# Kernel optimization log

Hardware: AMD Instinct MI355X
Metric: run time of the kernel (lower is better)

## Reference

```python
import jax, jax.numpy as jnp
import numpy as np

N0, N1, N2 = 65536, 8192, 1024   # node counts per depth (pool factor 8, as in original m1*2=8)
DEG = 6                          # avg degree of k-space neighbor graphs
K = 10                           # number of Gaussian kernels in GMMConv


def _pool_graph(n_fine):
    # bidirectional edges between each group of 8 nodes and its representative (last node of group)
    mem = jnp.arange(n_fine)
    rep = (mem // 8) * 8 + 7
    return jnp.concatenate([mem, rep]), jnp.concatenate([rep, mem])


def setup_inputs() -> dict:
    key = jax.random.key(0)
    ks = list(jax.random.split(key, 40))
    E1, E2, E3 = DEG * N0, DEG * N1, DEG * N2
    d = {}
    d['n_feat'] = jax.random.normal(ks[0], (N0, 2), jnp.float32)
    d['src1'] = jax.random.randint(ks[1], (E1,), 0, N0)
    d['dst1'] = jax.random.randint(ks[2], (E1,), 0, N0)
    d['pkor1'] = 0.5 * jax.random.normal(ks[3], (E1, 2), jnp.float32)
    d['src2'] = jax.random.randint(ks[4], (E2,), 0, N1)
    d['dst2'] = jax.random.randint(ks[5], (E2,), 0, N1)
    d['pkor2'] = 0.5 * jax.random.normal(ks[6], (E2, 2), jnp.float32)
    d['src3'] = jax.random.randint(ks[7], (E3,), 0, N2)
    d['dst3'] = jax.random.randint(ks[8], (E3,), 0, N2)
    d['pkor3'] = 0.5 * jax.random.normal(ks[9], (E3, 2), jnp.float32)
    d['pm1_src'], d['pm1_dst'] = _pool_graph(N0)
    d['pm2_src'], d['pm2_dst'] = _pool_graph(N1)
    d['idx1'] = jnp.arange(N1) * 8 + 7
    d['idx2'] = jnp.arange(N2) * 8 + 7

    def lin(k, fi, fo):
        return jax.random.normal(k, (fi, K * fo), jnp.float32) / np.float32(np.sqrt(fi * K))

    d['W1'] = lin(ks[10], 2, 32)
    d['mu1'] = jax.random.normal(ks[11], (K, 2), jnp.float32)
    d['is1'] = jax.random.uniform(ks[12], (K, 2), jnp.float32, 0.5, 1.5)
    d['b1'] = 0.01 * jax.random.normal(ks[13], (32,), jnp.float32)
    d['W2'] = lin(ks[14], 32, 64)
    d['mu2'] = jax.random.normal(ks[15], (K, 2), jnp.float32)
    d['is2'] = jax.random.uniform(ks[16], (K, 2), jnp.float32, 0.5, 1.5)
    d['W3'] = lin(ks[17], 64, 128)
    d['mu3'] = jax.random.normal(ks[18], (K, 2), jnp.float32)
    d['is3'] = jax.random.uniform(ks[19], (K, 2), jnp.float32, 0.5, 1.5)
    d['W4'] = lin(ks[20], 192, 64)
    d['mu4'] = jax.random.normal(ks[21], (K, 2), jnp.float32)
    d['is4'] = jax.random.uniform(ks[22], (K, 2), jnp.float32, 0.5, 1.5)
    d['W5'] = lin(ks[23], 96, 40)
    d['mu5'] = jax.random.normal(ks[24], (K, 2), jnp.float32)
    d['is5'] = jax.random.uniform(ks[25], (K, 2), jnp.float32, 0.5, 1.5)
    d['b5'] = 0.01 * jax.random.normal(ks[26], (40,), jnp.float32)
    return d


def gmm_conv(x, W, mu, inv_sigma, src, dst, pseudo, n, bias=None):
    # DGL GMMConv, aggregator 'mean': h=fc(x) -> (N,K,F); gaussian edge weights over 2D pseudo coords
    h = (x @ W).reshape(x.shape[0], K, -1)                                   # (N,K,F)
    diff = pseudo[:, None, :] - mu[None, :, :]                               # (E,K,2)
    gw = jnp.exp(-0.5 * jnp.sum(diff * diff * (inv_sigma[None] ** 2), -1))   # (E,K)
    msg = h[src] * gw[:, :, None]                                            # (E,K,F)
    s = jax.ops.segment_sum(msg, dst, num_segments=n)
    deg = jax.ops.segment_sum(jnp.ones(dst.shape, x.dtype), dst, num_segments=n)
    out = jnp.sum(s / jnp.maximum(deg, 1.0)[:, None, None], axis=1)          # mean over edges, sum over kernels
    return out if bias is None else out + bias


def max_reduce(h, src, dst, n):
    # DGL update_all(copy_u, max): nodes with no in-edges get 0
    m = jax.ops.segment_max(h[src], dst, num_segments=n)
    deg = jax.ops.segment_sum(jnp.ones(dst.shape, h.dtype), dst, num_segments=n)
    return jnp.where(deg[:, None] > 0, m, jnp.zeros((), h.dtype))


def reference(n_feat, src1, dst1, pkor1, src2, dst2, pkor2, src3, dst3, pkor3,
              pm1_src, pm1_dst, pm2_src, pm2_dst, idx1, idx2,
              W1, mu1, is1, b1, W2, mu2, is2, W3, mu3, is3,
              W4, mu4, is4, W5, mu5, is5, b5):
    # encoder
    out0 = jax.nn.relu(gmm_conv(n_feat, W1, mu1, is1, src1, dst1, pkor1, N0, b1))      # (N0,32) skip0
    h = max_reduce(out0, pm1_src, pm1_dst, N0)[idx1]                                    # MaxPool -> (N1,32)
    out1 = jax.nn.relu(gmm_conv(h, W2, mu2, is2, src2, dst2, pkor2, N1))                # (N1,64) skip1
    h = max_reduce(out1, pm2_src, pm2_dst, N1)[idx2]                                    # MaxPool -> (N2,64)
    out2 = jax.nn.relu(gmm_conv(h, W3, mu3, is3, src3, dst3, pkor3, N2))                # (N2,128) bottleneck
    # decoder
    hu = jnp.zeros((N1, out2.shape[1]), out2.dtype).at[idx2].set(out2)
    hu = max_reduce(hu, pm2_src, pm2_dst, N1)                                           # UpSample -> (N1,128)
    out3 = jax.nn.relu(gmm_conv(jnp.concatenate([hu, out1], 1), W4, mu4, is4,
                                src2, dst2, pkor2, N1))                                 # (N1,64)
    hu = jnp.zeros((N0, out3.shape[1]), out3.dtype).at[idx1].set(out3)
    hu = max_reduce(hu, pm1_src, pm1_dst, N0)                                           # UpSample -> (N0,64)
    return jnp.tanh(gmm_conv(jnp.concatenate([hu, out0], 1), W5, mu5, is5,
                             src1, dst1, pkor1, N0, b5))                                # (N0,40)
```

## Files before the change

### kernel.cpp

```cpp
#include <hip/hip_runtime.h>


#define N0C 65536
#define N1C 8192
#define N2C 1024
#define KK 10

typedef _Float16 half2t __attribute__((ext_vector_type(2)));
typedef _Float16 half4 __attribute__((ext_vector_type(4)));
typedef _Float16 f16x8 __attribute__((ext_vector_type(8)));
typedef float f32x4 __attribute__((ext_vector_type(4)));

static inline int cdiv(long long a, long long b) { return (int)((a + b - 1) / b); }

__device__ __forceinline__ size_t fragi(int r, int kd, int KDT) {
    return ((size_t)(r >> 4) * KDT + (kd >> 5)) * 64 + ((kd >> 3) & 3) * 16 + (r & 15);
}


__global__ __launch_bounds__(256)
void k_hist3(const int* __restrict__ d1, const int* __restrict__ d2,
             const int* __restrict__ d3, int* __restrict__ g1,
             int* __restrict__ g2, int* __restrict__ g3,
             int E1, int E2, int E3) {
    int i = blockIdx.x * 256 + threadIdx.x;
    if (i < E1) atomicAdd(&g1[d1[i]], 1);
    else if (i < E1 + E2) atomicAdd(&g2[d2[i - E1]], 1);
    else if (i < E1 + E2 + E3) atomicAdd(&g3[d3[i - E1 - E2]], 1);
}

__device__ __forceinline__ void map_graph(int b, int& lb, int& gi) {
    if (b < 256) { gi = 0; lb = b; }
    else if (b < 288) { gi = 1; lb = b - 256; }
    else { gi = 2; lb = b - 288; }
}

__global__ __launch_bounds__(256)
void k_scanall(const int* __restrict__ deg1, int* __restrict__ off1, float* __restrict__ inv1,
               const int* __restrict__ deg2, int* __restrict__ off2, float* __restrict__ inv2,
               const int* __restrict__ deg3, int* __restrict__ off3, float* __restrict__ inv3,
               int E1, int E2, int E3) {
    __shared__ int s[256];
    int lb, gi; map_graph(blockIdx.x, lb, gi);
    const int* deg = gi == 0 ? deg1 : (gi == 1 ? deg2 : deg3);
    int* off = gi == 0 ? off1 : (gi == 1 ? off2 : off3);
    float* inv = gi == 0 ? inv1 : (gi == 1 ? inv2 : inv3);
    int n = gi == 0 ? N0C : (gi == 1 ? N1C : N2C);
    int E = gi == 0 ? E1 : (gi == 1 ? E2 : E3);
    int pre = 0;
    for (int i = threadIdx.x; i < lb * 256; i += 256) pre += deg[i];
    s[threadIdx.x] = pre;
    __syncthreads();
#pragma unroll
    for (int d = 128; d > 0; d >>= 1) {
        if (threadIdx.x < d) s[threadIdx.x] += s[threadIdx.x + d];
        __syncthreads();
    }
    int base = s[0];
    __syncthreads();
    int i = lb * 256 + threadIdx.x;
    int v = deg[i];
    s[threadIdx.x] = v;
    __syncthreads();
#pragma unroll
    for (int d = 1; d < 256; d <<= 1) {
        int t = (threadIdx.x >= d) ? s[threadIdx.x - d] : 0;
        __syncthreads();
        s[threadIdx.x] += t;
        __syncthreads();
    }
    off[i] = base + s[threadIdx.x] - v;
    inv[i] = 1.0f / fmaxf((float)v, 1.0f);
    if (i == n - 1) off[n] = E;
}

__global__ __launch_bounds__(256)
void k_scatter3(const int* __restrict__ s1, const int* __restrict__ d1,
                const float* __restrict__ p1, const int* __restrict__ o1,
                int* __restrict__ c1, int* __restrict__ cs1, float2* __restrict__ cp1,
                const int* __restrict__ s2, const int* __restrict__ d2,
                const float* __restrict__ p2, const int* __restrict__ o2,
                int* __restrict__ c2, int* __restrict__ cs2, float2* __restrict__ cp2,
                const int* __restrict__ s3, const int* __restrict__ d3,
                const float* __restrict__ p3, const int* __restrict__ o3,
                int* __restrict__ c3, int* __restrict__ cs3, float2* __restrict__ cp3,
                int E1, int E2, int E3) {
    int i = blockIdx.x * 256 + threadIdx.x;
    const int* src; const int* dst; const float* pk; const int* off;
    int* cur; int* csrc; float2* cpk; int e;
    if (i < E1) { src = s1; dst = d1; pk = p1; off = o1; cur = c1; csrc = cs1; cpk = cp1; e = i; }
    else if (i < E1 + E2) { src = s2; dst = d2; pk = p2; off = o2; cur = c2; csrc = cs2; cpk = cp2; e = i - E1; }
    else if (i < E1 + E2 + E3) { src = s3; dst = d3; pk = p3; off = o3; cur = c3; csrc = cs3; cpk = cp3; e = i - E1 - E2; }
    else return;
    int d = dst[e];
    int p = off[d] + atomicAdd(&cur[d], 1);
    csrc[p] = src[e];
    cpk[p] = reinterpret_cast<const float2*>(pk)[e];
}

__global__ __launch_bounds__(256)
void k_gw(const float2* __restrict__ cp1, const float2* __restrict__ cp2,
          const float2* __restrict__ cp3,
          const float* __restrict__ mu1, const float* __restrict__ is1,
          const float* __restrict__ mu5, const float* __restrict__ is5,
          const float* __restrict__ mu2, const float* __restrict__ is2,
          const float* __restrict__ mu4, const float* __restrict__ is4,
          const float* __restrict__ mu3, const float* __restrict__ is3,
          float* __restrict__ g1, float* __restrict__ g5, float* __restrict__ g2,
          float* __restrict__ g4, float* __restrict__ g3,
          int E1, int E2, int E3) {
    int i = blockIdx.x * 256 + threadIdx.x;
    const float2* cp; const float* mu; const float* isg; float* g; int e;
    if (i < E1) { cp = cp1; mu = mu1; isg = is1; g = g1; e = i; }
    else if (i < 2 * E1) { cp = cp1; mu = mu5; isg = is5; g = g5; e = i - E1; }
    else if (i < 2 * E1 + E2) { cp = cp2; mu = mu2; isg = is2; g = g2; e = i - 2 * E1; }
    else if (i < 2 * E1 + 2 * E2) { cp = cp2; mu = mu4; isg = is4; g = g4; e = i - 2 * E1 - E2; }
    else if (i < 2 * E1 + 2 * E2 + E3) { cp = cp3; mu = mu3; isg = is3; g = g3; e = i - 2 * E1 - 2 * E2; }
    else return;
    float2 pk = cp[e];
    float o[KK];
#pragma unroll
    for (int k = 0; k < KK; ++k) {
        float dx = (pk.x - mu[2 * k]) * isg[2 * k];
        float dy = (pk.y - mu[2 * k + 1]) * isg[2 * k + 1];
        o[k] = __expf(-0.5f * (dx * dx + dy * dy));
    }
    float4* gp = reinterpret_cast<float4*>(g + (size_t)e * 12);
    gp[0] = make_float4(o[0], o[1], o[2], o[3]);
    gp[1] = make_float4(o[4], o[5], o[6], o[7]);
    gp[2] = make_float4(o[8], o[9], 0.f, 0.f);
}

#define LOAD_G2(gwp, j, G)                                                   \
    {                                                                        \
        const float4* gp_ = reinterpret_cast<const float4*>((gwp) + (size_t)(j) * 12); \
        float4 g0_ = gp_[0], g1_ = gp_[1];                                   \
        float2 g2_ = *reinterpret_cast<const float2*>(gp_ + 2);              \
        G[0] = g0_.x; G[1] = g0_.y; G[2] = g0_.z; G[3] = g0_.w;              \
        G[4] = g1_.x; G[5] = g1_.y; G[6] = g1_.z; G[7] = g1_.w;              \
        G[8] = g2_.x; G[9] = g2_.y;                                          \
    }

__global__ __launch_bounds__(256)
void k_prep_wt(const float* __restrict__ W1, const float* __restrict__ W2,
               const float* __restrict__ W3, const float* __restrict__ W4,
               const float* __restrict__ W5,
               _Float16* __restrict__ T2,
               _Float16* __restrict__ T3, _Float16* __restrict__ T4,
               _Float16* __restrict__ T5, int* __restrict__ degs, int degn) {
    int id = blockIdx.x * 256 + threadIdx.x;
    if (id < degn) degs[id] = 0;
    if (id < 20480) {
        int f = id / 320, kc = id % 320;
        T2[fragi(f, kc, 10) * 8 + (kc & 7)] = (_Float16)W2[(kc % 32) * 640 + (kc / 32) * 64 + f];
        return;
    }
    id -= 20480;
    if (id < 81920) {
        int f = id / 640, kc = id % 640;
        T3[fragi(f, kc, 20) * 8 + (kc & 7)] = (_Float16)W3[(kc % 64) * 1280 + (kc / 64) * 128 + f];
        return;
    }
    id -= 81920;
    if (id < 122880) {
        int f = id / 1920, kc = id % 1920;
        T4[fragi(f, kc, 60) * 8 + (kc & 7)] = (_Float16)W4[(kc % 192) * 640 + (kc / 192) * 64 + f];
        return;
    }
    id -= 122880;
    if (id < 46080) {
        int f = id / 960, kc = id % 960;
        float v = (f < 40) ? W5[(kc % 96) * 400 + (kc / 96) * 40 + f] : 0.0f;
        T5[fragi(f, kc, 30) * 8 + (kc & 7)] = (_Float16)v;
    }
}

__global__ __launch_bounds__(256, 3)
void k_l1(const float* __restrict__ x, const int* __restrict__ off,
          const int* __restrict__ csrc, const float* __restrict__ gw,
          const float* __restrict__ inv, const float* __restrict__ W1,
          const float* __restrict__ b1, _Float16* __restrict__ out0,
          _Float16* __restrict__ hp1) {
    __shared__ float Ws[640];
    __shared__ float bs[32];
    for (int i = threadIdx.x; i < 640; i += 256) Ws[i] = W1[i];
    if (threadIdx.x < 32) bs[threadIdx.x] = b1[threadIdx.x];
    __syncthreads();
    int tid2 = blockIdx.x * 256 + threadIdx.x;
    int n = tid2 >> 1;
    int h = tid2 & 1;
    float a0[KK], a1[KK];
#pragma unroll
    for (int k = 0; k < KK; ++k) { a0[k] = 0.f; a1[k] = 0.f; }
    int j0 = off[n], j1 = off[n + 1];
    int j = j0 + h;
    bool have = j < j1;
    float Gc[KK]; float2 xc;
    if (have) {
        int s = csrc[j];
        LOAD_G2(gw, j, Gc)
        xc = reinterpret_cast<const float2*>(x)[s];
    }
    while (have) {
        int jn = j + 2;
        bool hn = jn < j1;
        float Gn[KK]; float2 xn;
        if (hn) {
            int s = csrc[jn];
            LOAD_G2(gw, jn, Gn)
            xn = reinterpret_cast<const float2*>(x)[s];
        }
#pragma unroll
        for (int k = 0; k < KK; ++k) {
            a0[k] = fmaf(Gc[k], xc.x, a0[k]);
            a1[k] = fmaf(Gc[k], xc.y, a1[k]);
        }
        j = jn; have = hn;
        if (hn) {
#pragma unroll
            for (int k = 0; k < KK; ++k) Gc[k] = Gn[k];
            xc = xn;
        }
    }
    float iv = inv[n];
#pragma unroll
    for (int k = 0; k < KK; ++k) {
        a0[k] = (a0[k] + __shfl_xor(a0[k], 1)) * iv;
        a1[k] = (a1[k] + __shfl_xor(a1[k], 1)) * iv;
    }
    _Float16* orow = out0 + (size_t)n * 32;
    _Float16* prow = hp1 + (size_t)(tid2 >> 4) * 32;
#pragma unroll
    for (int t = 0; t < 4; ++t) {
        int f4 = h * 4 + t;
        float v0 = bs[f4 * 4], v1 = bs[f4 * 4 + 1], v2 = bs[f4 * 4 + 2], v3 = bs[f4 * 4 + 3];
#pragma unroll
        for (int k = 0; k < KK; ++k) {
            const float* w0 = Ws + k * 32 + f4 * 4;
            const float* w1 = w0 + 320;
            v0 += a0[k] * w0[0] + a1[k] * w1[0];
            v1 += a0[k] * w0[1] + a1[k] * w1[1];
            v2 += a0[k] * w0[2] + a1[k] * w1[2];
            v3 += a0[k] * w0[3] + a1[k] * w1[3];
        }
        v0 = fmaxf(v0, 0.f); v1 = fmaxf(v1, 0.f);
        v2 = fmaxf(v2, 0.f); v3 = fmaxf(v3, 0.f);
        half4 o;
        o[0] = (_Float16)v0; o[1] = (_Float16)v1;
        o[2] = (_Float16)v2; o[3] = (_Float16)v3;
        *reinterpret_cast<half4*>(orow + f4 * 4) = o;
#pragma unroll
        for (int d = 2; d < 16; d <<= 1) {
            v0 = fmaxf(v0, __shfl_xor(v0, d));
            v1 = fmaxf(v1, __shfl_xor(v1, d));
            v2 = fmaxf(v2, __shfl_xor(v2, d));
            v3 = fmaxf(v3, __shfl_xor(v3, d));
        }
        if ((threadIdx.x & 15) == h) {
            half4 p;
            p[0] = (_Float16)v0; p[1] = (_Float16)v1;
            p[2] = (_Float16)v2; p[3] = (_Float16)v3;
            *reinterpret_cast<half4*>(prow + f4 * 4) = p;
        }
    }
}

template <int TPN, int ES>
__global__ __launch_bounds__(256, 3)
void k_aggx(const _Float16* __restrict__ xp, const int* __restrict__ off,
            const int* __restrict__ csrc, const float* __restrict__ gw,
            const float* __restrict__ inv, _Float16* __restrict__ agg, int N) {
    constexpr int CIN = TPN * 4;
    constexpr int KDT = KK * CIN / 32;
    constexpr int TG = TPN * ES;
    int gtid = blockIdx.x * 256 + threadIdx.x;
    int node = gtid / TG;
    int rem = threadIdx.x % TG;
    int tt = rem % TPN, es = rem / TPN;
    if (node >= N) return;
    float a[KK][4];
#pragma unroll
    for (int k = 0; k < KK; ++k)
#pragma unroll
        for (int e = 0; e < 4; ++e) a[k][e] = 0.f;
    int j0 = off[node], j1 = off[node + 1];
    const _Float16* xb = xp + 4 * tt;
    int j = j0 + es;
    bool have = j < j1;
    float Gc[KK]; half4 hc;
    if (have) {
        int s = csrc[j];
        LOAD_G2(gw, j, Gc)
        hc = *reinterpret_cast<const half4*>(xb + (size_t)s * CIN);
    }
    while (have) {
        int jn = j + ES;
        bool hn = jn < j1;
        float Gn[KK]; half4 hx;
        if (hn) {
            int s = csrc[jn];
            LOAD_G2(gw, jn, Gn)
            hx = *reinterpret_cast<const half4*>(xb + (size_t)s * CIN);
        }
        float f0 = hc[0], f1 = hc[1], f2 = hc[2], f3 = hc[3];
#pragma unroll
        for (int k = 0; k < KK; ++k) {
            a[k][0] = fmaf(Gc[k], f0, a[k][0]);
            a[k][1] = fmaf(Gc[k], f1, a[k][1]);
            a[k][2] = fmaf(Gc[k], f2, a[k][2]);
            a[k][3] = fmaf(Gc[k], f3, a[k][3]);
        }
        j = jn; have = hn;
        if (hn) {
#pragma unroll
            for (int k = 0; k < KK; ++k) Gc[k] = Gn[k];
            hc = hx;
        }
    }
#pragma unroll
    for (int d = TPN; d < TG; d <<= 1)
#pragma unroll
        for (int k = 0; k < KK; ++k) {
            a[k][0] += __shfl_xor(a[k][0], d);
            a[k][1] += __shfl_xor(a[k][1], d);
            a[k][2] += __shfl_xor(a[k][2], d);
            a[k][3] += __shfl_xor(a[k][3], d);
        }
    if (es == 0) {
        float iv = inv[node];
#pragma unroll
        for (int k = 0; k < KK; ++k) {
            half4 o;
            o[0] = (_Float16)(a[k][0] * iv); o[1] = (_Float16)(a[k][1] * iv);
            o[2] = (_Float16)(a[k][2] * iv); o[3] = (_Float16)(a[k][3] * iv);
            int kd = k * CIN + 4 * tt;
            *reinterpret_cast<half4*>(agg + fragi(node, kd, KDT) * 8 + (kd & 7)) = o;
        }
    }
}

template <int CA, int CB, int WPB, int NPW, int NT, int ACT, int FST, int OUTH>
__global__ __launch_bounds__(WPB * 64)
void k_aggf4(const _Float16* __restrict__ xA, const _Float16* __restrict__ xB,
             const int* __restrict__ off, const int* __restrict__ csrc,
             const float* __restrict__ gw, const float* __restrict__ inv,
             const _Float16* __restrict__ Wt, const float* __restrict__ bias,
             void* __restrict__ outv, int nodeBase) {
    constexpr int CIN = CA + CB;
    constexpr int PAIRS = CIN / 2;
    constexpr int P = (PAIRS + 63) / 64;
    constexpr int KDT = KK * CIN / 32;
    constexpr int STRIDE = KK * CIN + 8;
    __shared__ _Float16 lds[16 * STRIDE];
    const int lane = threadIdx.x & 63;
    const int wv = threadIdx.x >> 6;
    int j0u[NPW], degu[NPW], sallu[NPW];
#pragma unroll
    for (int u = 0; u < NPW; ++u) {
        const int node = __builtin_amdgcn_readfirstlane(nodeBase + blockIdx.x * 16 + wv * NPW + u);
        j0u[u] = __builtin_amdgcn_readfirstlane(off[node]);
        int j1 = __builtin_amdgcn_readfirstlane(off[node + 1]);
        degu[u] = j1 - j0u[u];
        int pl = (degu[u] > 0) ? (j0u[u] + (lane < degu[u] ? lane : degu[u] - 1)) : 0;
        sallu[u] = csrc[pl];
    }

#define AGG_FMA(GA, GB, XA0, XA1, XB0, XB1)                                   \
    _Pragma("unroll")                                                         \
    for (int k_ = 0; k_ < KK; ++k_)                                           \
        _Pragma("unroll")                                                     \
        for (int p_ = 0; p_ < P; ++p_) {                                      \
            a[k_][2 * p_] = fmaf(GA[k_], XA0[p_], a[k_][2 * p_]);             \
            a[k_][2 * p_ + 1] = fmaf(GA[k_], XA1[p_], a[k_][2 * p_ + 1]);     \
            a[k_][2 * p_] = fmaf(GB[k_], XB0[p_], a[k_][2 * p_]);             \
            a[k_][2 * p_ + 1] = fmaf(GB[k_], XB1[p_], a[k_][2 * p_ + 1]);     \
        }

#pragma unroll
    for (int u = 0; u < NPW; ++u) {
        const int nl = wv * NPW + u;
        const int node = __builtin_amdgcn_readfirstlane(nodeBase + blockIdx.x * 16 + nl);
        const int j0 = j0u[u];
        const int deg = degu[u];
        const int sall = sallu[u];
        float a[KK][2 * P];
#pragma unroll
        for (int k = 0; k < KK; ++k)
#pragma unroll
            for (int p = 0; p < 2 * P; ++p) a[k][p] = 0.f;
        int e = 0;
        for (; e + 1 < deg; e += 2) {
            int sa = __builtin_amdgcn_readlane(sall, e);
            int sb = __builtin_amdgcn_readlane(sall, e + 1);
            int gj = __builtin_amdgcn_readfirstlane(j0 + e);
            float Ga[KK], Gb[KK];
            LOAD_G2(gw, gj, Ga)
            LOAD_G2(gw, gj + 1, Gb)
            float xa0[P], xa1[P], xb0[P], xb1[P];
#pragma unroll
            for (int p = 0; p < P; ++p) {
                int c0 = 2 * (lane + 64 * p);
                xa0[p] = 0.f; xa1[p] = 0.f; xb0[p] = 0.f; xb1[p] = 0.f;
                if (c0 < CIN) {
                    bool useA = c0 < CA;
                    const _Float16* qa = useA ? (xA + (size_t)(sa >> 3) * CA + c0)
                                              : (xB + (size_t)sa * CB + (c0 - CA));
                    const _Float16* qb = useA ? (xA + (size_t)(sb >> 3) * CA + c0)
                                              : (xB + (size_t)sb * CB + (c0 - CA));
                    half2t ha = *reinterpret_cast<const half2t*>(qa);
                    half2t hb = *reinterpret_cast<const half2t*>(qb);
                    xa0[p] = ha[0]; xa1[p] = ha[1];
                    xb0[p] = hb[0]; xb1[p] = hb[1];
                }
            }
            AGG_FMA(Ga, Gb, xa0, xa1, xb0, xb1)
        }
        if (e < deg) {
            int sa = __builtin_amdgcn_readlane(sall, e);
            int gj = __builtin_amdgcn_readfirstlane(j0 + e);
            float Ga[KK];
            LOAD_G2(gw, gj, Ga)
            float xa0[P], xa1[P];
#pragma unroll
            for (int p = 0; p < P; ++p) {
                int c0 = 2 * (lane + 64 * p);
                xa0[p] = 0.f; xa1[p] = 0.f;
                if (c0 < CIN) {
                    const _Float16* qa = (c0 < CA) ? (xA + (size_t)(sa >> 3) * CA + c0)
                                                   : (xB + (size_t)sa * CB + (c0 - CA));
                    half2t ha = *reinterpret_cast<const half2t*>(qa);
                    xa0[p] = ha[0]; xa1[p] = ha[1];
                }
            }
#pragma unroll
            for (int k = 0; k < KK; ++k)
#pragma unroll
                for (int p = 0; p < P; ++p) {
                    a[k][2 * p] = fmaf(Ga[k], xa0[p], a[k][2 * p]);
                    a[k][2 * p + 1] = fmaf(Ga[k], xa1[p], a[k][2 * p + 1]);
                }
        }
        float iv = inv[node];
#pragma unroll
        for (int k = 0; k < KK; ++k)
#pragma unroll
            for (int p = 0; p < P; ++p) {
                int c0 = 2 * (lane + 64 * p);
                if (c0 < CIN) {
                    half2t o;
                    o[0] = (_Float16)(a[k][2 * p] * iv);
                    o[1] = (_Float16)(a[k][2 * p + 1] * iv);
                    *reinterpret_cast<half2t*>(&lds[nl * STRIDE + k * CIN + c0]) = o;
                }
            }
    }
#undef AGG_FMA
    constexpr int PF = (KDT < 8) ? KDT : 8;
    const int lm = lane & 15;
    const int q = lane >> 4;
    const f16x8* bp = (const f16x8*)Wt + (size_t)wv * KDT * 64 + lane;
    f16x8 bfr[PF];
    if (wv < NT) {
#pragma unroll
        for (int i = 0; i < PF; ++i) bfr[i] = bp[(size_t)i * 64];
    }
    __syncthreads();
    if (wv < NT) {
        f32x4 acc = (f32x4){0.f, 0.f, 0.f, 0.f};
        f16x8 af = *reinterpret_cast<const f16x8*>(&lds[lm * STRIDE + q * 8]);
#pragma unroll
        for (int i = 0; i < KDT; ++i) {
            f16x8 afn;
            if (i + 1 < KDT)
                afn = *reinterpret_cast<const f16x8*>(&lds[lm * STRIDE + (i + 1) * 32 + q * 8]);
            f16x8 b = bfr[i % PF];
            if (i + PF < KDT) bfr[i % PF] = bp[(size_t)(i + PF) * 64];
            acc = __builtin_amdgcn_mfma_f32_16x16x32_f16(af, b, acc, 0, 0, 0);
            af = afn;
        }
        int f = wv * 16 + lm;
        if (f < FST) {
            float b = bias ? bias[f] : 0.0f;
#pragma unroll
            for (int r = 0; r < 4; ++r) {
                size_t node = (size_t)nodeBase + (size_t)blockIdx.x * 16 + q * 4 + r;
                float v = acc[r] + b;
                v = (ACT == 1) ? tanhf(v) : fmaxf(v, 0.0f);
                if (OUTH) ((_Float16*)outv)[node * FST + f] = (_Float16)v;
                else ((float*)outv)[node * FST + f] = v;
            }
        }
    }
}

template <int WB, int NT, int ITERS, int ACT, int FST, int OUTH, int POOL>
__global__ __launch_bounds__(WB * 64)
void k_gemm2(const _Float16* __restrict__ A, const _Float16* __restrict__ B,
             const float* __restrict__ bias, void* __restrict__ outv,
             _Float16* __restrict__ poolout, int M) {
    constexpr int KDT = ITERS;
    const int lane = threadIdx.x & 63;
    const int wv = threadIdx.x >> 6;
    const int lm = lane & 15;
    const int q = lane >> 4;
    const size_t m0 = (size_t)blockIdx.y * (WB * 16) + wv * 16;
    const size_t mblk = m0 >> 4;
    f32x4 acc[NT];
#pragma unroll
    for (int t = 0; t < NT; ++t) acc[t] = (f32x4){0.f, 0.f, 0.f, 0.f};
    const f16x8* ap = (const f16x8*)A + mblk * KDT * 64 + lane;
    const f16x8* bp = (const f16x8*)B + lane;
    f16x8 af = ap[0];
    f16x8 bf[NT];
#pragma unroll
    for (int t = 0; t < NT; ++t) bf[t] = bp[(size_t)t * KDT * 64];
#pragma unroll
    for (int i = 0; i < ITERS; ++i) {
        f16x8 afn; f16x8 bfn[NT];
        if (i + 1 < ITERS) {
            afn = ap[(size_t)(i + 1) * 64];
#pragma unroll
            for (int t = 0; t < NT; ++t)
                bfn[t] = bp[((size_t)t * KDT + i + 1) * 64];
        }
#pragma unroll
        for (int t = 0; t < NT; ++t)
            acc[t] = __builtin_amdgcn_mfma_f32_16x16x32_f16(af, bf[t], acc[t], 0, 0, 0);
        af = afn;
#pragma unroll
        for (int t = 0; t < NT; ++t) bf[t] = bfn[t];
    }
#pragma unroll
    for (int t = 0; t < NT; ++t) {
        int f = t * 16 + lm;
        if (f < FST) {
            float b = bias ? bias[f] : 0.0f;
            float vr[4];
#pragma unroll
            for (int r = 0; r < 4; ++r) {
                float v = acc[t][r] + b;
                vr[r] = (ACT == 1) ? tanhf(v) : fmaxf(v, 0.0f);
            }
#pragma unroll
            for (int r = 0; r < 4; ++r) {
                if (OUTH) ((_Float16*)outv)[(m0 + q * 4 + r) * (size_t)FST + f] = (_Float16)vr[r];
                else ((float*)outv)[(m0 + q * 4 + r) * (size_t)FST + f] = vr[r];
            }
            if (POOL) {
                float m = fmaxf(fmaxf(vr[0], vr[1]), fmaxf(vr[2], vr[3]));
                m = fmaxf(m, __shfl_xor(m, 16));
                if ((q & 1) == 0)
                    poolout[(size_t)((m0 >> 3) + (q >> 1)) * FST + f] = (_Float16)m;
            }
        }
    }
}

extern "C" void kernel_launch(void* const* d_in, const int* in_sizes, int n_in,
                              void* d_out, int out_size, void* d_ws, size_t ws_size,
                              hipStream_t stream) {
    const float* n_feat = (const float*)d_in[0];
    const int* src1 = (const int*)d_in[1];
    const int* dst1 = (const int*)d_in[2];
    const float* pkor1 = (const float*)d_in[3];
    const int* src2 = (const int*)d_in[4];
    const int* dst2 = (const int*)d_in[5];
    const float* pkor2 = (const float*)d_in[6];
    const int* src3 = (const int*)d_in[7];
    const int* dst3 = (const int*)d_in[8];
    const float* pkor3 = (const float*)d_in[9];
    const float* W1 = (const float*)d_in[16];
    const float* mu1 = (const float*)d_in[17];
    const float* is1 = (const float*)d_in[18];
    const float* b1 = (const float*)d_in[19];
    const float* W2 = (const float*)d_in[20];
    const float* mu2 = (const float*)d_in[21];
    const float* is2 = (const float*)d_in[22];
    const float* W3 = (const float*)d_in[23];
    const float* mu3 = (const float*)d_in[24];
    const float* is3 = (const float*)d_in[25];
    const float* W4 = (const float*)d_in[26];
    const float* mu4 = (const float*)d_in[27];
    const float* is4 = (const float*)d_in[28];
    const float* W5 = (const float*)d_in[29];
    const float* mu5 = (const float*)d_in[30];
    const float* is5 = (const float*)d_in[31];
    const float* b5 = (const float*)d_in[32];

    const int E1 = in_sizes[1], E2 = in_sizes[4], E3 = in_sizes[7];
    const int NT_ = N0C + N1C + N2C;

    char* w = (char*)d_ws;
    auto alloc = [&](size_t bytes) {
        void* p = (void*)w;
        w += (bytes + 255) & ~(size_t)255;
        return p;
    };
    int* degs = (int*)alloc((size_t)NT_ * 2 * 4);
    int* deg1 = degs, *deg2 = degs + N0C, *deg3 = degs + N0C + N1C;
    int* cur1 = degs + NT_, *cur2 = cur1 + N0C, *cur3 = cur2 + N1C;
    int* off1 = (int*)alloc(((size_t)N0C + 1) * 4);
    int* off2 = (int*)alloc(((size_t)N1C + 1) * 4);
    int* off3 = (int*)alloc(((size_t)N2C + 1) * 4);
    int* csrc1 = (int*)alloc((size_t)E1 * 4);
    float2* cpk1 = (float2*)alloc((size_t)E1 * 8);
    int* csrc2 = (int*)alloc((size_t)E2 * 4);
    float2* cpk2 = (float2*)alloc((size_t)E2 * 8);
    int* csrc3 = (int*)alloc((size_t)E3 * 4);
    float2* cpk3 = (float2*)alloc((size_t)E3 * 8);
    float* inv1 = (float*)alloc((size_t)N0C * 4);
    float* inv2 = (float*)alloc((size_t)N1C * 4);
    float* inv3 = (float*)alloc((size_t)N2C * 4);
    float* g1 = (float*)alloc(((size_t)2 * E1 + 2 * E2 + E3) * 12 * 4);
    float* g5 = g1 + (size_t)E1 * 12;
    float* g2 = g5 + (size_t)E1 * 12;
    float* g4 = g2 + (size_t)E2 * 12;
    float* g3 = g4 + (size_t)E2 * 12;
    _Float16* out0 = (_Float16*)alloc((size_t)N0C * 32 * 2);
    _Float16* out1 = (_Float16*)alloc((size_t)N1C * 64 * 2);
    _Float16* out2 = (_Float16*)alloc((size_t)N2C * 128 * 2);
    _Float16* out3 = (_Float16*)alloc((size_t)N1C * 64 * 2);
    _Float16* hp1 = (_Float16*)alloc((size_t)N1C * 32 * 2);
    _Float16* hp2 = (_Float16*)alloc((size_t)N2C * 64 * 2);
    _Float16* agg2 = (_Float16*)alloc((size_t)N1C * 320 * 2);
    _Float16* agg3 = (_Float16*)alloc((size_t)N2C * 640 * 2);
    _Float16* Wt2 = (_Float16*)alloc((size_t)64 * 320 * 2);
    _Float16* Wt3 = (_Float16*)alloc((size_t)128 * 640 * 2);
    _Float16* Wt4 = (_Float16*)alloc((size_t)64 * 1920 * 2);
    _Float16* Wt5 = (_Float16*)alloc((size_t)48 * 960 * 2);

    const int ET = E1 + E2 + E3;
    const int GT = 2 * E1 + 2 * E2 + E3;

    k_prep_wt<<<cdiv(271360, 256), 256, 0, stream>>>(W1, W2, W3, W4, W5,
                                                     Wt2, Wt3, Wt4, Wt5,
                                                     degs, NT_ * 2);
    k_hist3<<<cdiv(ET, 256), 256, 0, stream>>>(dst1, dst2, dst3, deg1, deg2, deg3, E1, E2, E3);
    k_scanall<<<292, 256, 0, stream>>>(deg1, off1, inv1, deg2, off2, inv2,
                                       deg3, off3, inv3, E1, E2, E3);
    k_scatter3<<<cdiv(ET, 256), 256, 0, stream>>>(
        src1, dst1, pkor1, off1, cur1, csrc1, cpk1,
        src2, dst2, pkor2, off2, cur2, csrc2, cpk2,
        src3, dst3, pkor3, off3, cur3, csrc3, cpk3, E1, E2, E3);
    k_gw<<<cdiv(GT, 256), 256, 0, stream>>>(
        cpk1, cpk2, cpk3, mu1, is1, mu5, is5, mu2, is2, mu4, is4, mu3, is3,
        g1, g5, g2, g4, g3, E1, E2, E3);

    k_l1<<<N0C * 2 / 256, 256, 0, stream>>>(n_feat, off1, csrc1, g1, inv1, W1, b1, out0, hp1);

    k_aggx<8, 2><<<cdiv((size_t)N1C * 16, 256), 256, 0, stream>>>(hp1, off2, csrc2, g2, inv2, agg2, N1C);
    k_gemm2<2, 4, 10, 0, 64, 1, 1><<<dim3(1, N1C / 32), 128, 0, stream>>>(agg2, Wt2, nullptr, out1, hp2, N1C);

    k_aggx<16, 4><<<cdiv((size_t)N2C * 64, 256), 256, 0, stream>>>(hp2, off3, csrc3, g3, inv3, agg3, N2C);
    k_gemm2<1, 8, 20, 0, 128, 1, 0><<<dim3(1, N2C / 16), 64, 0, stream>>>(agg3, Wt3, nullptr, out2, nullptr, N2C);

    k_aggf4<128, 64, 16, 1, 4, 0, 64, 1><<<N1C / 16, 1024, 0, stream>>>(
        out2, out1, off2, csrc2, g4, inv2, Wt4, nullptr, out3, 0);

    k_aggf4<64, 32, 8, 2, 3, 1, 40, 0><<<N0C / 16, 512, 0, stream>>>(
        out3, out0, off1, csrc1, g5, inv1, Wt5, b5, d_out, 0);
}
```

Before: 324.9 us.

## Sort nodes by degree for load-balanced aggregation in fused aggf4 kernels

Builds a degree histogram while the scan runs, then a degree-bucketed permutation of nodes for the two largest graphs during scatter. The fused aggregation+GEMM kernels process nodes in permuted order, so each 16-node tile has similar degrees and waves inside a block diverge less. The cost is extra atomics, a serial prefix loop over up to 63 bins per thread in scatter, and scattered output writes and input reads through the permutation.

```diff
diff --git a/kernel.cpp b/kernel.cpp
--- a/kernel.cpp
+++ b/kernel.cpp
@@ -39,7 +39,7 @@
 void k_scanall(const int* __restrict__ deg1, int* __restrict__ off1, float* __restrict__ inv1,
                const int* __restrict__ deg2, int* __restrict__ off2, float* __restrict__ inv2,
                const int* __restrict__ deg3, int* __restrict__ off3, float* __restrict__ inv3,
-               int E1, int E2, int E3) {
+               int* __restrict__ bins, int E1, int E2, int E3) {
     __shared__ int s[256];
     int lb, gi; map_graph(blockIdx.x, lb, gi);
     const int* deg = gi == 0 ? deg1 : (gi == 1 ? deg2 : deg3);
@@ -60,6 +60,8 @@
     __syncthreads();
     int i = lb * 256 + threadIdx.x;
     int v = deg[i];
+    if (gi == 0) atomicAdd(&bins[v < 63 ? v : 63], 1);
+    else if (gi == 1) atomicAdd(&bins[64 + (v < 63 ? v : 63)], 1);
     s[threadIdx.x] = v;
     __syncthreads();
 #pragma unroll
@@ -84,18 +86,38 @@
                 const int* __restrict__ s3, const int* __restrict__ d3,
                 const float* __restrict__ p3, const int* __restrict__ o3,
                 int* __restrict__ c3, int* __restrict__ cs3, float2* __restrict__ cp3,
+                const int* __restrict__ deg1, const int* __restrict__ deg2,
+                int* __restrict__ bins, int* __restrict__ perm1, int* __restrict__ perm2,
                 int E1, int E2, int E3) {
     int i = blockIdx.x * 256 + threadIdx.x;
-    const int* src; const int* dst; const float* pk; const int* off;
-    int* cur; int* csrc; float2* cpk; int e;
-    if (i < E1) { src = s1; dst = d1; pk = p1; off = o1; cur = c1; csrc = cs1; cpk = cp1; e = i; }
-    else if (i < E1 + E2) { src = s2; dst = d2; pk = p2; off = o2; cur = c2; csrc = cs2; cpk = cp2; e = i - E1; }
-    else if (i < E1 + E2 + E3) { src = s3; dst = d3; pk = p3; off = o3; cur = c3; csrc = cs3; cpk = cp3; e = i - E1 - E2; }
-    else return;
-    int d = dst[e];
-    int p = off[d] + atomicAdd(&cur[d], 1);
-    csrc[p] = src[e];
-    cpk[p] = reinterpret_cast<const float2*>(pk)[e];
+    {
+        const int* src; const int* dst; const float* pk; const int* off;
+        int* cur; int* csrc; float2* cpk; int e; bool have = true;
+        if (i < E1) { src = s1; dst = d1; pk = p1; off = o1; cur = c1; csrc = cs1; cpk = cp1; e = i; }
+        else if (i < E1 + E2) { src = s2; dst = d2; pk = p2; off = o2; cur = c2; csrc = cs2; cpk = cp2; e = i - E1; }
+        else if (i < E1 + E2 + E3) { src = s3; dst = d3; pk = p3; off = o3; cur = c3; csrc = cs3; cpk = cp3; e = i - E1 - E2; }
+        else have = false;
+        if (have) {
+            int d = dst[e];
+            int p = off[d] + atomicAdd(&cur[d], 1);
+            csrc[p] = src[e];
+            cpk[p] = reinterpret_cast<const float2*>(pk)[e];
+        }
+    }
+    if (i < N0C) {
+        int d = deg1[i]; if (d > 63) d = 63;
+        int boff = 0;
+        for (int b = 0; b < d; ++b) boff += bins[b];
+        int pos = boff + atomicAdd(&bins[128 + d], 1);
+        perm1[pos] = i;
+    }
+    if (i < N1C) {
+        int d = deg2[i]; if (d > 63) d = 63;
+        int boff = 0;
+        for (int b = 0; b < d; ++b) boff += bins[64 + b];
+        int pos = boff + atomicAdd(&bins[192 + d], 1);
+        perm2[pos] = i;
+    }
 }
 
 __global__ __launch_bounds__(256)
@@ -147,9 +169,11 @@
                const float* __restrict__ W5,
                _Float16* __restrict__ T2,
                _Float16* __restrict__ T3, _Float16* __restrict__ T4,
-               _Float16* __restrict__ T5, int* __restrict__ degs, int degn) {
+               _Float16* __restrict__ T5, int* __restrict__ degs, int degn,
+               int* __restrict__ bins) {
     int id = blockIdx.x * 256 + threadIdx.x;
     if (id < degn) degs[id] = 0;
+    if (id < 256) bins[id] = 0;
     if (id < 20480) {
         int f = id / 320, kc = id % 320;
         T2[fragi(f, kc, 10) * 8 + (kc & 7)] = (_Float16)W2[(kc % 32) * 640 + (kc / 32) * 64 + f];
@@ -345,7 +369,7 @@
              const int* __restrict__ off, const int* __restrict__ csrc,
              const float* __restrict__ gw, const float* __restrict__ inv,
              const _Float16* __restrict__ Wt, const float* __restrict__ bias,
-             void* __restrict__ outv, int nodeBase) {
+             void* __restrict__ outv, const int* __restrict__ perm, int nodeBase) {
     constexpr int CIN = CA + CB;
     constexpr int PAIRS = CIN / 2;
     constexpr int P = (PAIRS + 63) / 64;
@@ -354,12 +378,13 @@
     __shared__ _Float16 lds[16 * STRIDE];
     const int lane = threadIdx.x & 63;
     const int wv = threadIdx.x >> 6;
-    int j0u[NPW], degu[NPW], sallu[NPW];
+    const int tilebase = nodeBase + blockIdx.x * 16;
+    int j0u[NPW], degu[NPW], sallu[NPW], nodeu[NPW];
 #pragma unroll
     for (int u = 0; u < NPW; ++u) {
-        const int node = __builtin_amdgcn_readfirstlane(nodeBase + blockIdx.x * 16 + wv * NPW + u);
-        j0u[u] = __builtin_amdgcn_readfirstlane(off[node]);
-        int j1 = __builtin_amdgcn_readfirstlane(off[node + 1]);
+        nodeu[u] = __builtin_amdgcn_readfirstlane(perm[tilebase + wv * NPW + u]);
+        j0u[u] = __builtin_amdgcn_readfirstlane(off[nodeu[u]]);
+        int j1 = __builtin_amdgcn_readfirstlane(off[nodeu[u] + 1]);
         degu[u] = j1 - j0u[u];
         int pl = (degu[u] > 0) ? (j0u[u] + (lane < degu[u] ? lane : degu[u] - 1)) : 0;
         sallu[u] = csrc[pl];
@@ -379,7 +404,6 @@
 #pragma unroll
     for (int u = 0; u < NPW; ++u) {
         const int nl = wv * NPW + u;
-        const int node = __builtin_amdgcn_readfirstlane(nodeBase + blockIdx.x * 16 + nl);
         const int j0 = j0u[u];
         const int deg = degu[u];
         const int sall = sallu[u];
@@ -440,7 +464,7 @@
                     a[k][2 * p + 1] = fmaf(Ga[k], xa1[p], a[k][2 * p + 1]);
                 }
         }
-        float iv = inv[node];
+        float iv = inv[nodeu[u]];
 #pragma unroll
         for (int k = 0; k < KK; ++k)
 #pragma unroll
@@ -483,7 +507,7 @@
             float b = bias ? bias[f] : 0.0f;
 #pragma unroll
             for (int r = 0; r < 4; ++r) {
-                size_t node = (size_t)nodeBase + (size_t)blockIdx.x * 16 + q * 4 + r;
+                size_t node = (size_t)perm[tilebase + q * 4 + r];
                 float v = acc[r] + b;
                 v = (ACT == 1) ? tanhf(v) : fmaxf(v, 0.0f);
                 if (OUTH) ((_Float16*)outv)[node * FST + f] = (_Float16)v;
@@ -599,6 +623,9 @@
     int* degs = (int*)alloc((size_t)NT_ * 2 * 4);
     int* deg1 = degs, *deg2 = degs + N0C, *deg3 = degs + N0C + N1C;
     int* cur1 = degs + NT_, *cur2 = cur1 + N0C, *cur3 = cur2 + N1C;
+    int* bins = (int*)alloc(256 * 4);
+    int* perm1 = (int*)alloc((size_t)N0C * 4);
+    int* perm2 = (int*)alloc((size_t)N1C * 4);
     int* off1 = (int*)alloc(((size_t)N0C + 1) * 4);
     int* off2 = (int*)alloc(((size_t)N1C + 1) * 4);
     int* off3 = (int*)alloc(((size_t)N2C + 1) * 4);
@@ -634,14 +661,15 @@
 
     k_prep_wt<<<cdiv(271360, 256), 256, 0, stream>>>(W1, W2, W3, W4, W5,
                                                      Wt2, Wt3, Wt4, Wt5,
-                                                     degs, NT_ * 2);
+                                                     degs, NT_ * 2, bins);
     k_hist3<<<cdiv(ET, 256), 256, 0, stream>>>(dst1, dst2, dst3, deg1, deg2, deg3, E1, E2, E3);
     k_scanall<<<292, 256, 0, stream>>>(deg1, off1, inv1, deg2, off2, inv2,
-                                       deg3, off3, inv3, E1, E2, E3);
+                                       deg3, off3, inv3, bins, E1, E2, E3);
     k_scatter3<<<cdiv(ET, 256), 256, 0, stream>>>(
         src1, dst1, pkor1, off1, cur1, csrc1, cpk1,
         src2, dst2, pkor2, off2, cur2, csrc2, cpk2,
-        src3, dst3, pkor3, off3, cur3, csrc3, cpk3, E1, E2, E3);
+        src3, dst3, pkor3, off3, cur3, csrc3, cpk3,
+        deg1, deg2, bins, perm1, perm2, E1, E2, E3);
     k_gw<<<cdiv(GT, 256), 256, 0, stream>>>(
         cpk1, cpk2, cpk3, mu1, is1, mu5, is5, mu2, is2, mu4, is4, mu3, is3,
         g1, g5, g2, g4, g3, E1, E2, E3);
@@ -655,8 +683,8 @@
     k_gemm2<1, 8, 20, 0, 128, 1, 0><<<dim3(1, N2C / 16), 64, 0, stream>>>(agg3, Wt3, nullptr, out2, nullptr, N2C);
 
     k_aggf4<128, 64, 16, 1, 4, 0, 64, 1><<<N1C / 16, 1024, 0, stream>>>(
-        out2, out1, off2, csrc2, g4, inv2, Wt4, nullptr, out3, 0);
+        out2, out1, off2, csrc2, g4, inv2, Wt4, nullptr, out3, perm2, 0);
 
     k_aggf4<64, 32, 8, 2, 3, 1, 40, 0><<<N0C / 16, 512, 0, stream>>>(
-        out3, out0, off1, csrc1, g5, inv1, Wt5, b5, d_out, 0);
-}
+        out3, out0, off1, csrc1, g5, inv1, Wt5, b5, d_out, perm1, 0);
+}
```

New measurement: 769.9 us. 137% more time.
